# Kernel tuning notes

Measured on AMD Instinct MI355X. Metric: run time of the kernel, lower is better.

The kernel has to match this reference:

```python
import jax, jax.numpy as jnp
import numpy as np

EPS = 1e-7  # Keras K.epsilon()


def setup_inputs() -> dict:
    key = jax.random.key(0)
    k_x, k_w, k_b, k_u = jax.random.split(key, 4)
    B, T, D, A = 256, 512, 256, 50
    x = jax.random.normal(k_x, (B, T, D), dtype=jnp.float32)
    # Keras initializers.get('normal') -> stddev 0.05 RandomNormal
    W = jax.random.normal(k_w, (D, A), dtype=jnp.float32) * 0.05
    b = jax.random.normal(k_b, (A,), dtype=jnp.float32) * 0.05
    u = jax.random.normal(k_u, (A, 1), dtype=jnp.float32) * 0.05
    return {"x": x, "W": W, "b": b, "u": u}


def reference(x, W, b, u):
    # uit: [B, T, A]
    uit = jnp.tanh(jnp.einsum('btd,da->bta', x, W) + b)
    # ait: [B, T] raw scores -> exp-normalize (as in original, no max-subtract)
    ait = jnp.einsum('bta,a->bt', uit, u[:, 0])
    ait = jnp.exp(ait)
    ait = ait / (jnp.sum(ait, axis=1, keepdims=True) + EPS)
    # weighted pool over time: [B, D]
    return jnp.einsum('btd,bt->bd', x, ait)
```

## Files before the change

### kernel.cpp

```cpp
#include <hip/hip_runtime.h>
#include <math.h>

#define B_  256
#define T_  512
#define D_  256
#define A_  50
#define EPS 1e-7f

typedef short  short8  __attribute__((ext_vector_type(8)));
typedef float  floatx4 __attribute__((ext_vector_type(4)));

__device__ inline unsigned short f2bf(float f) {
    unsigned int u = __float_as_uint(f);
    u = (u + 0x7fffu + ((u >> 16) & 1u)) >> 16;
    return (unsigned short)u;
}

__global__ void prep_kernel(const float* __restrict__ W,
                            const float* __restrict__ bias,
                            const float* __restrict__ u,
                            unsigned short* __restrict__ Wf,
                            float* __restrict__ bu64)
{
    int idx = blockIdx.x * 256 + threadIdx.x;
    int j  = idx & 7;
    int l  = (idx >> 3) & 63;
    int ks = (idx >> 9) & 7;
    int nt = idx >> 12;
    int n  = nt * 16 + (l & 15);
    int k  = ks * 32 + (l >> 4) * 8 + j;
    float val = (n < A_) ? W[k * A_ + n] : 0.0f;
    Wf[idx] = f2bf(val);
    if (idx < 64) {
        bu64[idx]      = (idx < A_) ? bias[idx] : 0.0f;
        bu64[64 + idx] = (idx < A_) ? u[idx]    : 0.0f;
    }
}

__global__ __launch_bounds__(256)
void scores_kernel(const float* __restrict__ x,
                   const unsigned short* __restrict__ Wf,
                   const float* __restrict__ bu64,
                   float* __restrict__ s_out, float* __restrict__ partial)
{
    __shared__ float sred[64];

    const int tid  = threadIdx.x;
    const int w    = tid >> 6;
    const int l    = tid & 63;
    const int c    = l & 15;
    const int quad = l >> 4;
    const size_t rowbase = (size_t)blockIdx.x * 64 + w * 16;

    const float4* __restrict__ xrow = (const float4*)(x + (rowbase + c) * D_);
    const short8* __restrict__ wf8  = (const short8*)Wf;

    float bnc[4], unc[4];
    #pragma unroll
    for (int nt = 0; nt < 4; nt++) {
        bnc[nt] = bu64[nt * 16 + c];
        unc[nt] = bu64[64 + nt * 16 + c];
    }

    floatx4 acc[4];
    #pragma unroll
    for (int nt = 0; nt < 4; nt++) acc[nt] = (floatx4){0.f, 0.f, 0.f, 0.f};

    #pragma unroll
    for (int ks = 0; ks < 8; ks++) {
        const float4 a0 = xrow[ks * 8 + quad * 2];
        const float4 a1 = xrow[ks * 8 + quad * 2 + 1];
        short8 av;
        av[0] = (short)f2bf(a0.x); av[1] = (short)f2bf(a0.y);
        av[2] = (short)f2bf(a0.z); av[3] = (short)f2bf(a0.w);
        av[4] = (short)f2bf(a1.x); av[5] = (short)f2bf(a1.y);
        av[6] = (short)f2bf(a1.z); av[7] = (short)f2bf(a1.w);
        #pragma unroll
        for (int nt = 0; nt < 4; nt++) {
            const short8 bv = wf8[(nt * 8 + ks) * 64 + l];
            acc[nt] = __builtin_amdgcn_mfma_f32_16x16x32_bf16(av, bv, acc[nt], 0, 0, 0);
        }
    }

    float part[4];
    #pragma unroll
    for (int r = 0; r < 4; r++) {
        float v = 0.0f;
        #pragma unroll
        for (int nt = 0; nt < 4; nt++)
            v += tanhf(acc[nt][r] + bnc[nt]) * unc[nt];
        #pragma unroll
        for (int off = 1; off < 16; off <<= 1)
            v += __shfl_xor(v, off, 16);
        part[r] = v;
    }

    if (c == 0) {
        #pragma unroll
        for (int r = 0; r < 4; r++) {
            const float s = expf(part[r]);
            s_out[rowbase + quad * 4 + r] = s;
            sred[w * 16 + quad * 4 + r] = s;
        }
    }
    __syncthreads();
    if (tid == 0) {
        float s = 0.0f;
        #pragma unroll
        for (int i = 0; i < 64; i++) s += sred[i];
        partial[blockIdx.x] = s;
    }
}

__global__ __launch_bounds__(256)
void pool_kernel(const float* __restrict__ x, const float* __restrict__ s_in,
                 const float* __restrict__ partial, float* __restrict__ pp)
{
    __shared__ float s_lds[64];
    __shared__ float part[4 * 256];

    const int tid = threadIdx.x;
    const int bb  = blockIdx.x >> 3;
    const int q   = blockIdx.x & 7;

    float den = EPS;
    #pragma unroll
    for (int i = 0; i < 8; i++) den += partial[bb * 8 + i];
    const float inv = 1.0f / den;

    if (tid < 64)
        s_lds[tid] = s_in[(size_t)bb * T_ + q * 64 + tid] * inv;
    __syncthreads();

    const int w = tid >> 6;
    const int l = tid & 63;

    const float* __restrict__ xb = x + ((size_t)bb * T_ + q * 64) * D_;
    float4 acc = make_float4(0.f, 0.f, 0.f, 0.f);

    #pragma unroll
    for (int i = 0; i < 16; i++) {
        const int t = w * 16 + i;
        float4 xv = *(const float4*)(xb + (size_t)t * D_ + l * 4);
        float sv  = s_lds[t];
        acc.x += xv.x * sv;
        acc.y += xv.y * sv;
        acc.z += xv.z * sv;
        acc.w += xv.w * sv;
    }

    part[w * 256 + l * 4 + 0] = acc.x;
    part[w * 256 + l * 4 + 1] = acc.y;
    part[w * 256 + l * 4 + 2] = acc.z;
    part[w * 256 + l * 4 + 3] = acc.w;
    __syncthreads();

    pp[(size_t)blockIdx.x * 256 + tid] =
        part[tid] + part[256 + tid] + part[512 + tid] + part[768 + tid];
}

__global__ __launch_bounds__(256)
void combine_kernel(const float* __restrict__ pp, float* __restrict__ out)
{
    const size_t idx = (size_t)blockIdx.x * 256 + threadIdx.x;
    const size_t b   = idx >> 8;
    const size_t d   = idx & 255;
    float o = 0.0f;
    #pragma unroll
    for (int q = 0; q < 8; q++) o += pp[(b * 8 + q) * 256 + d];
    out[idx] = o;
}

extern "C" void kernel_launch(void* const* d_in, const int* in_sizes, int n_in,
                              void* d_out, int out_size, void* d_ws, size_t ws_size,
                              hipStream_t stream)
{
    const float* x = (const float*)d_in[0];
    const float* W = (const float*)d_in[1];
    const float* b = (const float*)d_in[2];
    const float* u = (const float*)d_in[3];

    float* scores  = (float*)d_ws;
    float* partial = scores + (size_t)B_ * T_;
    float* bu64    = partial + 2048;
    float* pp      = bu64 + 128;
    unsigned short* Wf = (unsigned short*)(pp + (size_t)B_ * 8 * 256);
    float* out     = (float*)d_out;

    prep_kernel   <<<64,   256, 0, stream>>>(W, b, u, Wf, bu64);
    scores_kernel <<<2048, 256, 0, stream>>>(x, Wf, bu64, scores, partial);
    pool_kernel   <<<2048, 256, 0, stream>>>(x, scores, partial, pp);
    combine_kernel<<<B_,   256, 0, stream>>>(pp, out);
}
```

Before: 224.4 us.

## Stage W in LDS, prefetch x rows, use fast tanh and packed bf16 convert

Several changes land in the scores kernel. The pre-swizzled bf16 W (32 KB) is copied into shared memory once per block, and all 16 float4 loads of the x row are issued up front. It also uses a hardware packed float-to-bf16 conversion, replaces tanhf with an exp-based fast tanh, and adds a launch-bounds occupancy hint. The goal is to cut per-MFMA global loads of W and the math cost in the epilogue, at the price of 32 KB of LDS per block, higher register pressure, and a small accuracy change from the fast tanh.

After: 219.9 us. 1.02x faster.

```diff
diff --git a/kernel.cpp b/kernel.cpp
--- a/kernel.cpp
+++ b/kernel.cpp
@@ -1,4 +1,5 @@
 #include <hip/hip_runtime.h>
+#include <hip/hip_bf16.h>
 #include <math.h>
 
 #define B_  256
@@ -14,6 +15,10 @@
     unsigned int u = __float_as_uint(f);
     u = (u + 0x7fffu + ((u >> 16) & 1u)) >> 16;
     return (unsigned short)u;
+}
+
+__device__ inline float tanh_fast(float v) {
+    return 1.0f - 2.0f / (__expf(2.0f * v) + 1.0f);
 }
 
 __global__ void prep_kernel(const float* __restrict__ W,
@@ -37,12 +42,25 @@
     }
 }
 
-__global__ __launch_bounds__(256)
+__device__ inline void pack_bf4(short8& av, int base, float fx, float fy,
+                                float fz, float fw)
+{
+    union { __hip_bfloat162 h2; int i; } c0, c1;
+    c0.h2 = __float22bfloat162_rn(make_float2(fx, fy));
+    c1.h2 = __float22bfloat162_rn(make_float2(fz, fw));
+    av[base + 0] = (short)(c0.i & 0xffff);
+    av[base + 1] = (short)((unsigned)c0.i >> 16);
+    av[base + 2] = (short)(c1.i & 0xffff);
+    av[base + 3] = (short)((unsigned)c1.i >> 16);
+}
+
+__global__ __launch_bounds__(256, 4)
 void scores_kernel(const float* __restrict__ x,
                    const unsigned short* __restrict__ Wf,
                    const float* __restrict__ bu64,
                    float* __restrict__ s_out, float* __restrict__ partial)
 {
+    __shared__ int4  Wl[2048];
     __shared__ float sred[64];
 
     const int tid  = threadIdx.x;
@@ -52,8 +70,15 @@
     const int quad = l >> 4;
     const size_t rowbase = (size_t)blockIdx.x * 64 + w * 16;
 
+    {
+        const int4* __restrict__ wsrc = (const int4*)Wf;
+        #pragma unroll
+        for (int i = 0; i < 8; i++)
+            Wl[tid + i * 256] = wsrc[tid + i * 256];
+    }
+
     const float4* __restrict__ xrow = (const float4*)(x + (rowbase + c) * D_);
-    const short8* __restrict__ wf8  = (const short8*)Wf;
+    const short8* __restrict__ wl8  = (const short8*)Wl;
 
     float bnc[4], unc[4];
     #pragma unroll
@@ -61,6 +86,12 @@
         bnc[nt] = bu64[nt * 16 + c];
         unc[nt] = bu64[64 + nt * 16 + c];
     }
+    __syncthreads();
+
+    float4 pre[16];
+    #pragma unroll
+    for (int i = 0; i < 16; i++)
+        pre[i] = xrow[(i >> 1) * 8 + quad * 2 + (i & 1)];
 
     floatx4 acc[4];
     #pragma unroll
@@ -68,37 +99,29 @@
 
     #pragma unroll
     for (int ks = 0; ks < 8; ks++) {
-        const float4 a0 = xrow[ks * 8 + quad * 2];
-        const float4 a1 = xrow[ks * 8 + quad * 2 + 1];
+        const float4 a0 = pre[2 * ks];
+        const float4 a1 = pre[2 * ks + 1];
         short8 av;
-        av[0] = (short)f2bf(a0.x); av[1] = (short)f2bf(a0.y);
-        av[2] = (short)f2bf(a0.z); av[3] = (short)f2bf(a0.w);
-        av[4] = (short)f2bf(a1.x); av[5] = (short)f2bf(a1.y);
-        av[6] = (short)f2bf(a1.z); av[7] = (short)f2bf(a1.w);
+        pack_bf4(av, 0, a0.x, a0.y, a0.z, a0.w);
+        pack_bf4(av, 4, a1.x, a1.y, a1.z, a1.w);
         #pragma unroll
         for (int nt = 0; nt < 4; nt++) {
-            const short8 bv = wf8[(nt * 8 + ks) * 64 + l];
+            const short8 bv = wl8[(nt * 8 + ks) * 64 + l];
             acc[nt] = __builtin_amdgcn_mfma_f32_16x16x32_bf16(av, bv, acc[nt], 0, 0, 0);
         }
     }
 
-    float part[4];
     #pragma unroll
     for (int r = 0; r < 4; r++) {
         float v = 0.0f;
         #pragma unroll
         for (int nt = 0; nt < 4; nt++)
-            v += tanhf(acc[nt][r] + bnc[nt]) * unc[nt];
+            v += tanh_fast(acc[nt][r] + bnc[nt]) * unc[nt];
         #pragma unroll
         for (int off = 1; off < 16; off <<= 1)
             v += __shfl_xor(v, off, 16);
-        part[r] = v;
-    }
-
-    if (c == 0) {
-        #pragma unroll
-        for (int r = 0; r < 4; r++) {
-            const float s = expf(part[r]);
+        if (c == 0) {
+            const float s = expf(v);
             s_out[rowbase + quad * 4 + r] = s;
             sred[w * 16 + quad * 4 + r] = s;
         }
```
